# Performance work log

Measured on AMD Instinct MI355X. Metric: run time of the kernel, lower is better.

## Reference

```python
import jax, jax.numpy as jnp
import numpy as np

B, T, I, H, O = 256, 512, 64, 512, 1


def _lstm_layer(x, Wih, Whh, bih, bhh):
    # x: [B, T, in]; Wih: [4H, in]; Whh: [4H, H]
    # Precompute input contribution for all timesteps (big GEMM, no recurrence).
    xg = jnp.einsum('bti,gi->btg', x, Wih) + bih + bhh  # [B, T, 4H]
    h0 = jnp.zeros((x.shape[0], Whh.shape[1]), x.dtype)
    c0 = jnp.zeros_like(h0)

    def step(carry, xt):
        h, c = carry
        gates = xt + h @ Whh.T  # [B, 4H]
        i, f, g, o = jnp.split(gates, 4, axis=-1)  # PyTorch gate order i,f,g,o
        i = jax.nn.sigmoid(i)
        f = jax.nn.sigmoid(f)
        g = jnp.tanh(g)
        o = jax.nn.sigmoid(o)
        c = f * c + i * g
        h = o * jnp.tanh(c)
        return (h, c), h

    _, hs = jax.lax.scan(step, (h0, c0), jnp.swapaxes(xg, 0, 1))  # [T, B, H]
    return jnp.swapaxes(hs, 0, 1)  # [B, T, H]


def setup_inputs() -> dict:
    key = jax.random.key(0)
    ks = jax.random.split(key, 12)
    s = 1.0 / np.sqrt(H)
    u = lambda k, shp: jax.random.uniform(k, shp, jnp.float32, -s, s)
    return {
        'x': jax.random.normal(ks[0], (B, T, I), jnp.float32),
        'Wih0': u(ks[1], (4 * H, I)),
        'Whh0': u(ks[2], (4 * H, H)),
        'bih0': u(ks[3], (4 * H,)),
        'bhh0': u(ks[4], (4 * H,)),
        'Wih1': u(ks[5], (4 * H, H)),
        'Whh1': u(ks[6], (4 * H, H)),
        'bih1': u(ks[7], (4 * H,)),
        'bhh1': u(ks[8], (4 * H,)),
        'Wfc': u(ks[9], (O, H)),
        'bfc': u(ks[10], (O,)),
    }


def reference(x, Wih0, Whh0, bih0, bhh0, Wih1, Whh1, bih1, bhh1, Wfc, bfc):
    h1 = _lstm_layer(x, Wih0, Whh0, bih0, bhh0)   # [B, T, H]
    h2 = _lstm_layer(h1, Wih1, Whh1, bih1, bhh1)  # [B, T, H]
    return h2[:, -1] @ Wfc.T + bfc  # [B, O]
```

## Files before the change

### kernel.cpp

```cpp
#include <hip/hip_runtime.h>

typedef unsigned short u16;
typedef unsigned long long u64;
typedef short bf16x8 __attribute__((ext_vector_type(8)));
typedef float f32x4 __attribute__((ext_vector_type(4)));

#define B_ 256
#define T_ 512
#define I_ 64
#define H_ 512
#define RING 32

#define OFF_F0    0u
#define OFF_F1    32768u
#define OFF_F2    65536u
#define OFF_F3    98304u
#define OFF_B0    131072u
#define OFF_B1    139264u
#define OFF_WIH0  147456u
#define OFF_WHH0  409600u
#define OFF_WIH1  2506752u
#define OFF_WHH1  4603904u
#define OFF_HX1   6701056u
#define OFF_H1R   7225344u
#define WS_NEEDED 15613952u

#define AQ __ATOMIC_RELAXED
#define SC __HIP_MEMORY_SCOPE_AGENT

static __device__ __forceinline__ u16 f2b(float f) {
  union { float f; unsigned u; } v; v.f = f;
  unsigned r = (v.u + 0x7FFFu + ((v.u >> 16) & 1u)) >> 16;
  return (u16)r;
}
static __device__ __forceinline__ float sigm(float x) { return 1.f / (1.f + __expf(-x)); }
static __device__ __forceinline__ float tanh_(float x) { return 1.f - 2.f / (__expf(2.f * x) + 1.f); }

static __device__ __forceinline__ void spin2(const unsigned* __restrict__ pa, unsigned tg) {
  unsigned a = __hip_atomic_load(pa, AQ, SC);
  for (;;) {
    unsigned b = __hip_atomic_load(pa, AQ, SC);
    if (!__any(a < tg)) break;
    a = __hip_atomic_load(pa, AQ, SC);
    if (!__any(b < tg)) break;
  }
  asm volatile("" ::: "memory");
}

__global__ void prep_kernel(const float* __restrict__ Wih0, const float* __restrict__ Whh0,
                            const float* __restrict__ bih0, const float* __restrict__ bhh0,
                            const float* __restrict__ Wih1, const float* __restrict__ Whh1,
                            const float* __restrict__ bih1, const float* __restrict__ bhh1,
                            const float* __restrict__ bfc, float* __restrict__ out,
                            char* __restrict__ ws) {
  unsigned* flags = (unsigned*)(ws + OFF_F0);
  float* b0 = (float*)(ws + OFF_B0);
  float* b1 = (float*)(ws + OFF_B1);
  u16* wih0b = (u16*)(ws + OFF_WIH0);
  u16* whh0b = (u16*)(ws + OFF_WHH0);
  u16* wih1b = (u16*)(ws + OFF_WIH1);
  u16* whh1b = (u16*)(ws + OFF_WHH1);

  long long i = (long long)blockIdx.x * 256 + threadIdx.x;
  if (i < 32768) { __hip_atomic_store(&flags[i], 0u, AQ, SC); return; }
  i -= 32768;
  if (i < 256) { out[i] = bfc[0]; return; }
  i -= 256;
  if (i < 2048) { b0[i] = bih0[i] + bhh0[i]; return; }
  i -= 2048;
  if (i < 2048) { b1[i] = bih1[i] + bhh1[i]; return; }
  i -= 2048;
  if (i < 131072) { wih0b[i] = f2b(Wih0[i]); return; }
  i -= 131072;
  if (i < 1048576) { whh0b[i] = f2b(Whh0[i]); return; }
  i -= 1048576;
  if (i < 1048576) { wih1b[i] = f2b(Wih1[i]); return; }
  i -= 1048576;
  if (i < 1048576) { whh1b[i] = f2b(Whh1[i]); return; }
}

template <bool IS_L0>
__device__ __forceinline__ void lstm_body(
    int ib, int jn,
    const float* __restrict__ x,
    const u16* __restrict__ Wib,
    const u16* __restrict__ Whb,
    const float* __restrict__ bias,
    unsigned* __restrict__ hx32,
    u16* __restrict__ h1ring,
    const float* __restrict__ Wfc, float* __restrict__ out,
    unsigned* __restrict__ fR,
    unsigned* __restrict__ fP,
    unsigned* __restrict__ fC,
    float* __restrict__ Gp_s)
{
  const int tid = threadIdx.x;
  const int wv = tid >> 6;
  const int lane = tid & 63;
  const int quad = lane >> 4;
  const int l15 = lane & 15;

  bf16x8 Bh[4][4];
#pragma unroll
  for (int r = 0; r < 4; ++r)
#pragma unroll
    for (int nt = 0; nt < 4; ++nt)
      Bh[r][nt] = *(const bf16x8*)&Whb[(size_t)(nt * 512 + jn * 16 + l15) * 512 +
                                       (wv * 4 + r) * 32 + quad * 8];
  bf16x8 Bx[4][4];
  bf16x8 Bx0[4];
  if constexpr (IS_L0) {
    if (wv < 2) {
#pragma unroll
      for (int nt = 0; nt < 4; ++nt)
        Bx0[nt] = *(const bf16x8*)&Wib[(size_t)(nt * 512 + jn * 16 + l15) * 64 +
                                       wv * 32 + quad * 8];
    }
  } else {
#pragma unroll
    for (int r = 0; r < 4; ++r)
#pragma unroll
      for (int nt = 0; nt < 4; ++nt)
        Bx[r][nt] = *(const bf16x8*)&Wib[(size_t)(nt * 512 + jn * 16 + l15) * 512 +
                                         (wv * 4 + r) * 32 + quad * 8];
  }

  const int erow = tid >> 3;
  const int ecp = tid & 7;
  float bias2[4][2];
#pragma unroll
  for (int g = 0; g < 4; ++g) {
    bias2[g][0] = bias[g * 512 + jn * 16 + 2 * ecp];
    bias2[g][1] = bias[g * 512 + jn * 16 + 2 * ecp + 1];
  }
  float cst2[2] = {0.f, 0.f};
  const f32x4 zf = {0.f, 0.f, 0.f, 0.f};
  const unsigned lineoff = ((unsigned)ib * 32 + jn) * 32;

  const int bg = ib * 32 + erow;
  const int hg = jn * 16 + 2 * ecp;
  const unsigned stoff = (unsigned)(((hg >> 3) * 256 + bg) * 4 + (ecp & 3));

  const unsigned* pollA = &fR[lineoff + (lane & 31)];
  const unsigned* pollB;
  if constexpr (IS_L0)
    pollB = &fC[lineoff + (lane & 31)];
  else
    pollB = &fP[lineoff + (lane & 31)];

  if constexpr (!IS_L0) {
    if (wv == 0) spin2(pollB, 1u);
  }

  for (int t = 0; t < T_; ++t) {
    f32x4 acc[2][4];
#pragma unroll
    for (int mt = 0; mt < 2; ++mt)
#pragma unroll
      for (int nt = 0; nt < 4; ++nt) acc[mt][nt] = zf;

    if constexpr (IS_L0) {
      if (wv < 2) {
        const float* xp = x + ((size_t)(ib * 32 + l15) * T_ + t) * 64 + wv * 32 + quad * 8;
        const float* xq = xp + (size_t)16 * T_ * 64;
        float4 xa = *(const float4*)xp;
        float4 xb = *(const float4*)(xp + 4);
        float4 xc = *(const float4*)xq;
        float4 xd = *(const float4*)(xq + 4);
        union { unsigned u[4]; bf16x8 v; } P0, P1;
        P0.u[0] = (unsigned)f2b(xa.x) | ((unsigned)f2b(xa.y) << 16);
        P0.u[1] = (unsigned)f2b(xa.z) | ((unsigned)f2b(xa.w) << 16);
        P0.u[2] = (unsigned)f2b(xb.x) | ((unsigned)f2b(xb.y) << 16);
        P0.u[3] = (unsigned)f2b(xb.z) | ((unsigned)f2b(xb.w) << 16);
        P1.u[0] = (unsigned)f2b(xc.x) | ((unsigned)f2b(xc.y) << 16);
        P1.u[1] = (unsigned)f2b(xc.z) | ((unsigned)f2b(xc.w) << 16);
        P1.u[2] = (unsigned)f2b(xd.x) | ((unsigned)f2b(xd.y) << 16);
        P1.u[3] = (unsigned)f2b(xd.z) | ((unsigned)f2b(xd.w) << 16);
#pragma unroll
        for (int nt = 0; nt < 4; ++nt) {
          acc[0][nt] = __builtin_amdgcn_mfma_f32_16x16x32_bf16(P0.v, Bx0[nt], acc[0][nt], 0, 0, 0);
          acc[1][nt] = __builtin_amdgcn_mfma_f32_16x16x32_bf16(P1.v, Bx0[nt], acc[1][nt], 0, 0, 0);
        }
      }
      __syncthreads();
    } else {
      __syncthreads();
      const u64* hq1 = (const u64*)h1ring + (size_t)(t & (RING - 1)) * (B_ * H_ / 4);
#pragma unroll
      for (int r = 0; r < 4; ++r) {
        int ks = wv * 4 + r;
        bf16x8 af[2];
#pragma unroll
        for (int mt = 0; mt < 2; ++mt) {
          const u64* p = hq1 + (size_t)((ks * 4 + quad) * 256 + ib * 32 + mt * 16 + l15) * 2;
          union { u64 q[2]; bf16x8 v; } u;
          u.q[0] = __hip_atomic_load(p, AQ, SC);
          u.q[1] = __hip_atomic_load(p + 1, AQ, SC);
          af[mt] = u.v;
        }
#pragma unroll
        for (int nt = 0; nt < 4; ++nt) {
          acc[0][nt] = __builtin_amdgcn_mfma_f32_16x16x32_bf16(af[0], Bx[r][nt], acc[0][nt], 0, 0, 0);
          acc[1][nt] = __builtin_amdgcn_mfma_f32_16x16x32_bf16(af[1], Bx[r][nt], acc[1][nt], 0, 0, 0);
        }
      }
    }

    __builtin_amdgcn_s_setprio(1);

    if (t) {
      const u64* hq;
      if constexpr (IS_L0)
        hq = (const u64*)h1ring + (size_t)((t - 1) & (RING - 1)) * (B_ * H_ / 4);
      else
        hq = (const u64*)hx32 + (size_t)(t & 1) * (B_ * H_ / 4);
      bf16x8 af[4][2];
#pragma unroll
      for (int r = 0; r < 4; ++r) {
        int ks = wv * 4 + r;
#pragma unroll
        for (int mt = 0; mt < 2; ++mt) {
          const u64* p = hq + (size_t)((ks * 4 + quad) * 256 + ib * 32 + mt * 16 + l15) * 2;
          union { u64 q[2]; bf16x8 v; } u;
          u.q[0] = __hip_atomic_load(p, AQ, SC);
          u.q[1] = __hip_atomic_load(p + 1, AQ, SC);
          af[r][mt] = u.v;
        }
      }
#pragma unroll
      for (int r = 0; r < 4; ++r)
#pragma unroll
        for (int mt = 0; mt < 2; ++mt)
#pragma unroll
          for (int nt = 0; nt < 4; ++nt)
            acc[mt][nt] = __builtin_amdgcn_mfma_f32_16x16x32_bf16(af[r][mt], Bh[r][nt],
                                                                  acc[mt][nt], 0, 0, 0);
    }

#pragma unroll
    for (int mt = 0; mt < 2; ++mt)
#pragma unroll
      for (int nt = 0; nt < 4; ++nt)
        *(f32x4*)&Gp_s[(nt * 16 + l15) * 132 + wv * 32 + mt * 16 + quad * 4] = acc[mt][nt];
    __syncthreads();

    {
      float pre[4][2];
#pragma unroll
      for (int g = 0; g < 4; ++g) {
#pragma unroll
        for (int j = 0; j < 2; ++j) {
          const int c = g * 16 + 2 * ecp + j;
          float s = bias2[g][j];
#pragma unroll
          for (int w = 0; w < 4; ++w) s += Gp_s[c * 132 + w * 32 + erow];
          pre[g][j] = s;
        }
      }
      float hv[2];
#pragma unroll
      for (int j = 0; j < 2; ++j) {
        float iv = sigm(pre[0][j]);
        float fv = sigm(pre[1][j]);
        float gv = tanh_(pre[2][j]);
        float ov = sigm(pre[3][j]);
        float cn = fv * cst2[j] + iv * gv;
        cst2[j] = cn;
        hv[j] = ov * tanh_(cn);
      }
      unsigned pack = (unsigned)f2b(hv[0]) | ((unsigned)f2b(hv[1]) << 16);
      if constexpr (IS_L0) {
        unsigned* ring32 = (unsigned*)h1ring;
        __hip_atomic_store(&ring32[(size_t)(t & (RING - 1)) * (B_ * H_ / 2) + stoff],
                           pack, AQ, SC);
      } else {
        __hip_atomic_store(&hx32[(size_t)((t + 1) & 1) * (B_ * H_ / 2) + stoff], pack, AQ, SC);
        if (t == T_ - 1) {
          float part = hv[0] * Wfc[hg] + hv[1] * Wfc[hg + 1];
          part += __shfl_down(part, 4, 8);
          part += __shfl_down(part, 2, 8);
          part += __shfl_down(part, 1, 8);
          if (ecp == 0) atomicAdd(&out[bg], part);
        }
      }
    }
    __builtin_amdgcn_s_setprio(0);

    __syncthreads();
    if (wv == 0) {
      unsigned val = (unsigned)(t + 1);
      if constexpr (IS_L0) {
        if (lane < 32)
          __hip_atomic_store(&fR[((unsigned)ib * 32 + lane) * 32 + jn], val, AQ, SC);
        else
          __hip_atomic_store(&fP[((unsigned)ib * 32 + (lane - 32)) * 32 + jn], val, AQ, SC);
      } else {
        if (lane < 32)
          __hip_atomic_store(&fR[((unsigned)ib * 32 + lane) * 32 + jn], val, AQ, SC);
        else
          __hip_atomic_store(&fC[((unsigned)ib * 32 + (lane - 32)) * 32 + jn], val, AQ, SC);
      }
      if (t + 1 < T_) {
        if constexpr (IS_L0) {
          const unsigned tg = (lane < 32)
              ? (unsigned)(t + 1)
              : ((t + 1 >= RING) ? (unsigned)(t + 2 - RING) : 0u);
          spin2((lane < 32) ? pollA : pollB, tg);
        } else {
          unsigned tP = (unsigned)(t + 2); if (tP > (unsigned)T_) tP = (unsigned)T_;
          const unsigned tg = (lane < 32) ? (unsigned)(t + 1) : tP;
          spin2((lane < 32) ? pollA : pollB, tg);
        }
      }
    }
  }
}

__global__ __launch_bounds__(256, 2) void lstm_fused(
    const float* __restrict__ x,
    const u16* __restrict__ wih0, const u16* __restrict__ whh0, const float* __restrict__ b0,
    const u16* __restrict__ wih1, const u16* __restrict__ whh1, const float* __restrict__ b1,
    unsigned* __restrict__ hx1, u16* __restrict__ h1ring,
    const float* __restrict__ Wfc, float* __restrict__ out,
    unsigned* __restrict__ f0, unsigned* __restrict__ f1, unsigned* __restrict__ f2,
    unsigned* __restrict__ f3)
{
  __shared__ __align__(16) float Gp_s[64 * 132];
  const int bx = blockIdx.x;
  if (bx < 256)
    lstm_body<true>(bx & 7, bx >> 3, x, wih0, whh0, b0, (unsigned*)nullptr, h1ring,
                    (const float*)nullptr, (float*)nullptr, f0, f1, f3, Gp_s);
  else
    lstm_body<false>((bx - 256) & 7, (bx - 256) >> 3, (const float*)nullptr, wih1, whh1, b1,
                     hx1, h1ring, Wfc, out, f2, f1, f3, Gp_s);
}

extern "C" void kernel_launch(void* const* d_in, const int* in_sizes, int n_in,
                              void* d_out, int out_size, void* d_ws, size_t ws_size,
                              hipStream_t stream) {
  if (ws_size < (size_t)WS_NEEDED) return;

  const float* x    = (const float*)d_in[0];
  const float* Wih0 = (const float*)d_in[1];
  const float* Whh0 = (const float*)d_in[2];
  const float* bih0 = (const float*)d_in[3];
  const float* bhh0 = (const float*)d_in[4];
  const float* Wih1 = (const float*)d_in[5];
  const float* Whh1 = (const float*)d_in[6];
  const float* bih1 = (const float*)d_in[7];
  const float* bhh1 = (const float*)d_in[8];
  const float* Wfc  = (const float*)d_in[9];
  const float* bfc  = (const float*)d_in[10];

  char* ws = (char*)d_ws;
  unsigned* f0   = (unsigned*)(ws + OFF_F0);
  unsigned* f1   = (unsigned*)(ws + OFF_F1);
  unsigned* f2   = (unsigned*)(ws + OFF_F2);
  unsigned* f3   = (unsigned*)(ws + OFF_F3);
  float* b0      = (float*)(ws + OFF_B0);
  float* b1      = (float*)(ws + OFF_B1);
  u16* wih0b     = (u16*)(ws + OFF_WIH0);
  u16* whh0b     = (u16*)(ws + OFF_WHH0);
  u16* wih1b     = (u16*)(ws + OFF_WIH1);
  u16* whh1b     = (u16*)(ws + OFF_WHH1);
  unsigned* hx1  = (unsigned*)(ws + OFF_HX1);
  u16* h1ring    = (u16*)(ws + OFF_H1R);
  float* out     = (float*)d_out;

  prep_kernel<<<12948, 256, 0, stream>>>(Wih0, Whh0, bih0, bhh0, Wih1, Whh1, bih1, bhh1,
                                         bfc, out, ws);

  lstm_fused<<<512, 256, 0, stream>>>(x, wih0b, whh0b, b0, wih1b, whh1b, b1,
                                      hx1, h1ring, Wfc, out, f0, f1, f2, f3);
}
```

Baseline: 2.886 ms.

## Prefetch next-step inputs and move spin-wait after input-projection MFMAs

Software-pipelines the per-step input operands: layer 0 loads the next timestep's x while the current one is consumed, and layer 1 loads the next step's h1 ring slice from global memory into registers ahead of time. The spin-wait on inter-block flags moves from the end of each step to just after the input-projection MFMAs, so that work overlaps with waiting for other blocks. The aim is to hide global-load latency and synchronisation latency on the serial recurrence path. In exchange it raises register pressure (pfa holds 8 bf16x8 fragments) and changes the ordering subtlety of the flag protocol.

```diff
diff --git a/kernel.cpp b/kernel.cpp
--- a/kernel.cpp
+++ b/kernel.cpp
@@ -148,8 +148,32 @@
   else
     pollB = &fP[lineoff + (lane & 31)];
 
-  if constexpr (!IS_L0) {
+  float4 xa, xb, xc, xd;
+  bf16x8 pfa[4][2];
+
+  if constexpr (IS_L0) {
+    if (wv < 2) {
+      const float* xp = x + ((size_t)(ib * 32 + l15) * T_) * 64 + wv * 32 + quad * 8;
+      const float* xq = xp + (size_t)16 * T_ * 64;
+      xa = *(const float4*)xp;  xb = *(const float4*)(xp + 4);
+      xc = *(const float4*)xq;  xd = *(const float4*)(xq + 4);
+    }
+  } else {
     if (wv == 0) spin2(pollB, 1u);
+    __syncthreads();
+    const u64* hq0 = (const u64*)h1ring;
+#pragma unroll
+    for (int r = 0; r < 4; ++r) {
+      int ks = wv * 4 + r;
+#pragma unroll
+      for (int mt = 0; mt < 2; ++mt) {
+        const u64* p = hq0 + (size_t)((ks * 4 + quad) * 256 + ib * 32 + mt * 16 + l15) * 2;
+        union { u64 q[2]; bf16x8 v; } u;
+        u.q[0] = __hip_atomic_load(p, AQ, SC);
+        u.q[1] = __hip_atomic_load(p + 1, AQ, SC);
+        pfa[r][mt] = u.v;
+      }
+    }
   }
 
   for (int t = 0; t < T_; ++t) {
@@ -161,12 +185,6 @@
 
     if constexpr (IS_L0) {
       if (wv < 2) {
-        const float* xp = x + ((size_t)(ib * 32 + l15) * T_ + t) * 64 + wv * 32 + quad * 8;
-        const float* xq = xp + (size_t)16 * T_ * 64;
-        float4 xa = *(const float4*)xp;
-        float4 xb = *(const float4*)(xp + 4);
-        float4 xc = *(const float4*)xq;
-        float4 xd = *(const float4*)(xq + 4);
         union { unsigned u[4]; bf16x8 v; } P0, P1;
         P0.u[0] = (unsigned)f2b(xa.x) | ((unsigned)f2b(xa.y) << 16);
         P0.u[1] = (unsigned)f2b(xa.z) | ((unsigned)f2b(xa.w) << 16);
@@ -181,27 +199,45 @@
           acc[0][nt] = __builtin_amdgcn_mfma_f32_16x16x32_bf16(P0.v, Bx0[nt], acc[0][nt], 0, 0, 0);
           acc[1][nt] = __builtin_amdgcn_mfma_f32_16x16x32_bf16(P1.v, Bx0[nt], acc[1][nt], 0, 0, 0);
         }
+        const int tn = (t + 1 < T_) ? t + 1 : t;
+        const float* xp = x + ((size_t)(ib * 32 + l15) * T_ + tn) * 64 + wv * 32 + quad * 8;
+        const float* xq = xp + (size_t)16 * T_ * 64;
+        xa = *(const float4*)xp;  xb = *(const float4*)(xp + 4);
+        xc = *(const float4*)xq;  xd = *(const float4*)(xq + 4);
+      }
+      if (t && wv == 0) {
+        const unsigned tg = (lane < 32) ? (unsigned)t
+                            : ((t >= RING) ? (unsigned)(t - RING + 1) : 0u);
+        spin2((lane < 32) ? pollA : pollB, tg);
       }
       __syncthreads();
     } else {
+#pragma unroll
+      for (int r = 0; r < 4; ++r)
+#pragma unroll
+        for (int nt = 0; nt < 4; ++nt) {
+          acc[0][nt] = __builtin_amdgcn_mfma_f32_16x16x32_bf16(pfa[r][0], Bx[r][nt], acc[0][nt], 0, 0, 0);
+          acc[1][nt] = __builtin_amdgcn_mfma_f32_16x16x32_bf16(pfa[r][1], Bx[r][nt], acc[1][nt], 0, 0, 0);
+        }
+      if (wv == 0) {
+        unsigned tP = (unsigned)(t + 2); if (tP > (unsigned)T_) tP = (unsigned)T_;
+        const unsigned tg = (lane < 32) ? (unsigned)t : tP;
+        spin2((lane < 32) ? pollA : pollB, tg);
+      }
       __syncthreads();
-      const u64* hq1 = (const u64*)h1ring + (size_t)(t & (RING - 1)) * (B_ * H_ / 4);
-#pragma unroll
-      for (int r = 0; r < 4; ++r) {
-        int ks = wv * 4 + r;
-        bf16x8 af[2];
-#pragma unroll
-        for (int mt = 0; mt < 2; ++mt) {
-          const u64* p = hq1 + (size_t)((ks * 4 + quad) * 256 + ib * 32 + mt * 16 + l15) * 2;
-          union { u64 q[2]; bf16x8 v; } u;
-          u.q[0] = __hip_atomic_load(p, AQ, SC);
-          u.q[1] = __hip_atomic_load(p + 1, AQ, SC);
-          af[mt] = u.v;
-        }
-#pragma unroll
-        for (int nt = 0; nt < 4; ++nt) {
-          acc[0][nt] = __builtin_amdgcn_mfma_f32_16x16x32_bf16(af[0], Bx[r][nt], acc[0][nt], 0, 0, 0);
-          acc[1][nt] = __builtin_amdgcn_mfma_f32_16x16x32_bf16(af[1], Bx[r][nt], acc[1][nt], 0, 0, 0);
+      if (t + 1 < T_) {
+        const u64* hq1n = (const u64*)h1ring + (size_t)((t + 1) & (RING - 1)) * (B_ * H_ / 4);
+#pragma unroll
+        for (int r = 0; r < 4; ++r) {
+          int ks = wv * 4 + r;
+#pragma unroll
+          for (int mt = 0; mt < 2; ++mt) {
+            const u64* p = hq1n + (size_t)((ks * 4 + quad) * 256 + ib * 32 + mt * 16 + l15) * 2;
+            union { u64 q[2]; bf16x8 v; } u;
+            u.q[0] = __hip_atomic_load(p, AQ, SC);
+            u.q[1] = __hip_atomic_load(p + 1, AQ, SC);
+            pfa[r][mt] = u.v;
+          }
         }
       }
     }
@@ -299,18 +335,6 @@
           __hip_atomic_store(&fR[((unsigned)ib * 32 + lane) * 32 + jn], val, AQ, SC);
         else
           __hip_atomic_store(&fC[((unsigned)ib * 32 + (lane - 32)) * 32 + jn], val, AQ, SC);
-      }
-      if (t + 1 < T_) {
-        if constexpr (IS_L0) {
-          const unsigned tg = (lane < 32)
-              ? (unsigned)(t + 1)
-              : ((t + 1 >= RING) ? (unsigned)(t + 2 - RING) : 0u);
-          spin2((lane < 32) ? pollA : pollB, tg);
-        } else {
-          unsigned tP = (unsigned)(t + 2); if (tP > (unsigned)T_) tP = (unsigned)T_;
-          const unsigned tg = (lane < 32) ? (unsigned)(t + 1) : tP;
-          spin2((lane < 32) ? pollA : pollB, tg);
-        }
       }
     }
   }
```

Result: faster. 2.529 ms (-12.4%).
